# Kernel optimization log

Hardware: AMD Instinct MI355X
Metric: run time of the kernel (lower is better)

The kernel has to match this reference:

```python
import jax, jax.numpy as jnp
import numpy as np

B, C, H, W = 16, 256, 64, 64
NH, HD, NM = 4, 32, 4  # heads, head_dim, memory tokens
HID = NH * HD


def rms_norm(x, g):
    # F.normalize(x, dim=1) * sqrt(C) * g  (channel dim = 1)
    norm = jnp.maximum(jnp.linalg.norm(x, axis=1, keepdims=True), 1e-12)
    return x / norm * (x.shape[1] ** 0.5) * g


def setup_inputs() -> dict:
    key = jax.random.key(0)
    ks = jax.random.split(key, 5)
    return {
        "x": jax.random.normal(ks[0], (B, C, H, W), jnp.float32),
        "g_in": jnp.ones((1, C, 1, 1), jnp.float32),
        "mem_kv": jax.random.normal(ks[1], (2, NH, HD, NM), jnp.float32),
        "w_qkv": jax.random.normal(ks[2], (HID * 3, C), jnp.float32) * (C ** -0.5),
        "w_out": jax.random.normal(ks[3], (C, HID), jnp.float32) * (HID ** -0.5),
        "b_out": jnp.zeros((C,), jnp.float32),
        "g_out": jnp.ones((1, C, 1, 1), jnp.float32),
    }


def reference(x, g_in, mem_kv, w_qkv, w_out, b_out, g_out):
    b, c, h, w = x.shape
    n = h * w
    scale = HD ** -0.5

    xn = rms_norm(x, g_in)
    # 1x1 conv as matmul over channel dim: [B, 3*HID, H, W]
    qkv = jnp.einsum('oc,bchw->bohw', w_qkv, xn)
    q, k, v = jnp.split(qkv, 3, axis=1)
    # b (h d) x y -> b h d n
    q = q.reshape(b, NH, HD, n)
    k = k.reshape(b, NH, HD, n)
    v = v.reshape(b, NH, HD, n)

    # prepend memory key/value tokens: [b, h, d, NM + n]
    mk = jnp.broadcast_to(mem_kv[0], (b, NH, HD, NM))
    mv = jnp.broadcast_to(mem_kv[1], (b, NH, HD, NM))
    k = jnp.concatenate([mk, k], axis=-1)
    v = jnp.concatenate([mv, v], axis=-1)

    q = jax.nn.softmax(q, axis=-2) * scale  # softmax over head_dim
    k = jax.nn.softmax(k, axis=-1)          # softmax over tokens

    context = jnp.einsum('bhdn,bhen->bhde', k, v)  # [b, h, d, e]
    out = jnp.einsum('bhde,bhdn->bhen', context, q)  # [b, h, e, n]
    out = out.reshape(b, HID, h, w)

    out = jnp.einsum('oc,bchw->bohw', w_out, out) + b_out[None, :, None, None]
    return rms_norm(out, g_out)
```

## Files before the change

### kernel.cpp

```cpp
#include <hip/hip_runtime.h>
#include <math.h>

typedef unsigned short u16;
typedef unsigned int u32;

#define NBATCH 16
#define NCH    256
#define NPIX   4096
#define NHEAD  4
#define HDIM   32
#define NMEM   4
#define HID    128
#define OC3    384
#define SCALE_Q 0.17677669529663687f

typedef __bf16 bf16x8 __attribute__((ext_vector_type(8)));
typedef float  f32x4  __attribute__((ext_vector_type(4)));

__device__ __forceinline__ float bf2f(u16 u){ return __uint_as_float(((u32)u)<<16); }
__device__ __forceinline__ u16 bfb(float f){
  union { __bf16 h; u16 u; } x; x.h = (__bf16)f; return x.u;
}
__device__ __forceinline__ u32 pkbf2(float a, float b){
  union { __bf16 h[2]; u32 u; } x; x.h[0] = (__bf16)a; x.h[1] = (__bf16)b; return x.u;
}
__device__ __forceinline__ void unpack8(int4 v, float* o){
  u32 a=(u32)v.x, b=(u32)v.y, c=(u32)v.z, d=(u32)v.w;
  o[0]=__uint_as_float(a<<16); o[1]=__uint_as_float(a&0xffff0000u);
  o[2]=__uint_as_float(b<<16); o[3]=__uint_as_float(b&0xffff0000u);
  o[4]=__uint_as_float(c<<16); o[5]=__uint_as_float(c&0xffff0000u);
  o[6]=__uint_as_float(d<<16); o[7]=__uint_as_float(d&0xffff0000u);
}
__device__ __forceinline__ void gload_lds16(const void* gp, void* lp){
  __builtin_amdgcn_global_load_lds(
      (const __attribute__((address_space(1))) unsigned int*)gp,
      (__attribute__((address_space(3))) unsigned int*)lp, 16, 0, 0);
}

__global__ __launch_bounds__(256) void k_pack(const float* __restrict__ wqkv,
                                              const float* __restrict__ gin,
                                              const float* __restrict__ wout,
                                              u16* __restrict__ wqb,
                                              u16* __restrict__ wob)
{
  int i = blockIdx.x*256 + threadIdx.x;
  if (i < OC3*NCH){ int c = i & 255; wqb[i] = bfb(wqkv[i]*gin[c]); }
  else { int j = i - OC3*NCH; wob[j] = bfb(wout[j]); }
}

__global__ __launch_bounds__(512, 4) void k_qkvx(const float* __restrict__ x,
                                                 const u16* __restrict__ wqb,
                                                 u16* __restrict__ qt,
                                                 u16* __restrict__ kv)
{
  __shared__ __align__(16) char smem[52480];
  float (*Xs)[64]   = (float(*)[64])smem;
  u16*   Bx         = (u16*)(smem + 16384);
  float (*ssqp)[64] = (float(*)[64])(smem + 50176);
  float* rl         = (float*)(smem + 52224);
  float (*psx)[64]  = (float(*)[64])smem;

  const int t = threadIdx.x, w = t>>6, lane = t&63;
  const int n0 = blockIdx.x*64, b = blockIdx.y;
  const int qw = lane>>4, rr = lane&15;

  {
    float ssq = 0.f;
    for (int s=0;s<4;++s){
      asm volatile("s_waitcnt lgkmcnt(0)" ::: "memory");
      const float* gp = x + ((size_t)b*NCH + s*64 + w*8 + (lane>>4))*NPIX + n0 + (lane&15)*4;
      gload_lds16(gp,                    &Xs[w*8 + 0][0]);
      gload_lds16(gp + (size_t)4*NPIX,   &Xs[w*8 + 4][0]);
      asm volatile("s_waitcnt vmcnt(0)" ::: "memory");
      u32 pk[4];
      #pragma unroll
      for (int q=0;q<4;q++){
        float v0 = Xs[w*8 + 2*q    ][lane];
        float v1 = Xs[w*8 + 2*q + 1][lane];
        ssq += v0*v0 + v1*v1;
        pk[q] = pkbf2(v0, v1);
      }
      *(int4*)&Bx[lane*264 + s*64 + w*8] = make_int4((int)pk[0],(int)pk[1],(int)pk[2],(int)pk[3]);
    }
    ssqp[w][lane] = ssq;
  }
  __syncthreads();
  if (t < 64){
    float s = 0.f;
    #pragma unroll
    for (int g=0;g<8;g++) s += ssqp[g][t];
    rl[t] = 16.0f / fmaxf(sqrtf(s), 1e-12f);
  }

  f32x4 acc[3][4];
  #pragma unroll
  for (int p=0;p<3;p++)
    #pragma unroll
    for (int nf=0;nf<4;nf++) acc[p][nf] = (f32x4){0.f,0.f,0.f,0.f};

  const u16* aw = wqb + (size_t)(w*16 + rr)*NCH + qw*8;
  bf16x8 caf0 = *(const bf16x8*)(aw);
  bf16x8 caf1 = *(const bf16x8*)(aw + 128*NCH);
  bf16x8 caf2 = *(const bf16x8*)(aw + 256*NCH);
  #pragma unroll
  for (int c0=0; c0<NCH; c0+=32){
    bf16x8 bfr[4];
    #pragma unroll
    for (int nf=0;nf<4;nf++)
      bfr[nf] = *(const bf16x8*)&Bx[(nf*16+rr)*264 + c0 + qw*8];
    bf16x8 naf0 = caf0, naf1 = caf1, naf2 = caf2;
    if (c0 < NCH-32){
      naf0 = *(const bf16x8*)(aw + c0+32);
      naf1 = *(const bf16x8*)(aw + 128*NCH + c0+32);
      naf2 = *(const bf16x8*)(aw + 256*NCH + c0+32);
    }
    #pragma unroll
    for (int nf=0;nf<4;nf++){
      acc[0][nf] = __builtin_amdgcn_mfma_f32_16x16x32_bf16(caf0, bfr[nf], acc[0][nf], 0, 0, 0);
      acc[1][nf] = __builtin_amdgcn_mfma_f32_16x16x32_bf16(bfr[nf], caf1, acc[1][nf], 0, 0, 0);
      acc[2][nf] = __builtin_amdgcn_mfma_f32_16x16x32_bf16(bfr[nf], caf2, acc[2][nf], 0, 0, 0);
    }
    caf0 = naf0; caf1 = naf1; caf2 = naf2;
  }

  __syncthreads();

  #pragma unroll
  for (int p=1;p<3;p++){
    u16* base = kv + ((size_t)(b*256 + (p-1)*128 + w*16 + rr))*NPIX + n0;
    #pragma unroll
    for (int nf=0;nf<4;nf++){
      const float4 rv4 = *(const float4*)&rl[nf*16 + qw*4];
      u32 lo = pkbf2(acc[p][nf][0]*rv4.x, acc[p][nf][1]*rv4.y);
      u32 hi = pkbf2(acc[p][nf][2]*rv4.z, acc[p][nf][3]*rv4.w);
      *(int2*)(base + nf*16 + qw*4) = make_int2((int)lo,(int)hi);
    }
  }

  float qv[4][4], pm[4], ps[4];
  #pragma unroll
  for (int nf=0;nf<4;nf++){
    float rv = rl[nf*16 + rr];
    float m = -1e30f;
    #pragma unroll
    for (int r=0;r<4;r++){ qv[nf][r] = acc[0][nf][r]*rv; m = fmaxf(m, qv[nf][r]); }
    m = fmaxf(m, __shfl_xor(m, 16, 64));
    m = fmaxf(m, __shfl_xor(m, 32, 64));
    float s = 0.f;
    #pragma unroll
    for (int r=0;r<4;r++){ qv[nf][r] = __expf(qv[nf][r]-m); s += qv[nf][r]; }
    s += __shfl_xor(s, 16, 64);
    s += __shfl_xor(s, 32, 64);
    pm[nf] = m; ps[nf] = s;
  }
  if (lane < 16){
    #pragma unroll
    for (int nf=0;nf<4;nf++){ ssqp[w][nf*16+lane] = pm[nf]; psx[w][nf*16+lane] = ps[nf]; }
  }
  __syncthreads();
  {
    const int pw = w^1;
    u16* qbase = qt + ((size_t)b*NPIX + n0)*HID + w*16 + qw*4;
    #pragma unroll
    for (int nf=0;nf<4;nf++){
      float om = ssqp[pw][nf*16+rr], os = psx[pw][nf*16+rr];
      float M = fmaxf(pm[nf], om);
      float S = ps[nf]*__expf(pm[nf]-M) + os*__expf(om-M);
      float f = __expf(pm[nf]-M) * SCALE_Q / S;
      u32 lo = pkbf2(qv[nf][0]*f, qv[nf][1]*f);
      u32 hi = pkbf2(qv[nf][2]*f, qv[nf][3]*f);
      *(int2*)(qbase + (size_t)(nf*16+rr)*HID) = make_int2((int)lo,(int)hi);
    }
  }
}

__global__ __launch_bounds__(256) void k_kred(const u16* __restrict__ kv,
                                              const float* __restrict__ memkv,
                                              float2* __restrict__ kms,
                                              float* __restrict__ ksm)
{
  const int rid = blockIdx.x*4 + (threadIdx.x>>6);
  const int lane = threadIdx.x & 63;
  const int d = rid & 31, h = (rid>>5)&3, b = rid>>7;
  const u16* p = kv + (size_t)(b*256 + h*HDIM + d)*NPIX;
  u32 buf[32];
  #pragma unroll
  for (int j=0;j<8;j++)
    *(int4*)&buf[j*4] = *(const int4*)(p + (size_t)(j*64+lane)*8);
  float m = -1e30f;
  #pragma unroll
  for (int i=0;i<32;i++){
    float lo = __uint_as_float(buf[i]<<16);
    float hi = __uint_as_float(buf[i]&0xffff0000u);
    m = fmaxf(m, fmaxf(lo, hi));
  }
  float mv[4];
  #pragma unroll
  for (int mm=0;mm<4;mm++){ mv[mm] = memkv[(h*HDIM+d)*NMEM + mm]; m = fmaxf(m, mv[mm]); }
  #pragma unroll
  for (int sh=1; sh<64; sh<<=1) m = fmaxf(m, __shfl_xor(m, sh, 64));
  float ssum = 0.f;
  #pragma unroll
  for (int i=0;i<32;i++){
    float lo = __uint_as_float(buf[i]<<16);
    float hi = __uint_as_float(buf[i]&0xffff0000u);
    ssum += __expf(lo-m) + __expf(hi-m);
  }
  #pragma unroll
  for (int sh=1; sh<64; sh<<=1) ssum += __shfl_xor(ssum, sh, 64);
  #pragma unroll
  for (int mm=0;mm<4;mm++) ssum += __expf(mv[mm]-m);
  float inv = 1.0f/ssum;
  if (lane==0) kms[rid] = make_float2(m, inv);
  if (lane<4) ksm[rid*NMEM + lane] = __expf(mv[lane]-m)*inv;
}

__global__ __launch_bounds__(64) void k_ctx(const u16* __restrict__ kv,
                                            const float* __restrict__ memkv,
                                            const float* __restrict__ ksm,
                                            const float2* __restrict__ kms,
                                            float* __restrict__ ctxp)
{
  __shared__ float Ks[32][68];
  __shared__ float Vs[32][68];
  const int bh = blockIdx.x;
  const int s  = blockIdx.y;
  const int b = bh>>2, h = bh&3;
  const int t = threadIdx.x;
  const int d0 = (t>>3)*4, e0 = (t&7)*4;
  float acc[4][4] = {};
  if (s==0){
    #pragma unroll
    for (int m=0;m<4;m++){
      float km[4];
      #pragma unroll
      for (int pi=0;pi<4;pi++) km[pi] = ksm[(bh*HDIM + d0+pi)*NMEM + m];
      #pragma unroll
      for (int q=0;q<4;q++){
        float vm = memkv[((NHEAD+h)*HDIM + e0+q)*NMEM + m];
        #pragma unroll
        for (int pi=0;pi<4;pi++) acc[pi][q] += km[pi]*vm;
      }
    }
  }
  const u16* kb = kv + (size_t)(b*256 +       h*HDIM)*NPIX;
  const u16* vb = kv + (size_t)(b*256 + HID + h*HDIM)*NPIX;
  const int lr = t>>1, lseg = (t&1)*32;
  const float2 ms = kms[bh*HDIM + lr];
  #pragma unroll
  for (int half=0; half<2; ++half){
    const int n0 = s*128 + half*64;
    const u16* kp = kb + (size_t)lr*NPIX + n0 + lseg;
    const u16* vp = vb + (size_t)lr*NPIX + n0 + lseg;
    #pragma unroll
    for (int u=0;u<4;u++){
      int4 kvv = *(const int4*)(kp + u*8);
      int4 vv  = *(const int4*)(vp + u*8);
      float kf[8], vf[8];
      unpack8(kvv,kf); unpack8(vv,vf);
      #pragma unroll
      for (int i=0;i<8;i++) kf[i] = __expf(kf[i]-ms.x)*ms.y;
      *(float4*)&Ks[lr][lseg+u*8]   = make_float4(kf[0],kf[1],kf[2],kf[3]);
      *(float4*)&Ks[lr][lseg+u*8+4] = make_float4(kf[4],kf[5],kf[6],kf[7]);
      *(float4*)&Vs[lr][lseg+u*8]   = make_float4(vf[0],vf[1],vf[2],vf[3]);
      *(float4*)&Vs[lr][lseg+u*8+4] = make_float4(vf[4],vf[5],vf[6],vf[7]);
    }
    __syncthreads();
    #pragma unroll 4
    for (int nn=0;nn<64;nn+=4){
      float kq[4][4] __attribute__((aligned(16)));
      float vq[4][4] __attribute__((aligned(16)));
      #pragma unroll
      for (int pi=0;pi<4;pi++) *(float4*)kq[pi] = *(const float4*)&Ks[d0+pi][nn];
      #pragma unroll
      for (int q=0;q<4;q++)    *(float4*)vq[q]  = *(const float4*)&Vs[e0+q][nn];
      #pragma unroll
      for (int pi=0;pi<4;pi++)
        #pragma unroll
        for (int q=0;q<4;q++)
          acc[pi][q] += kq[pi][0]*vq[q][0] + kq[pi][1]*vq[q][1]
                      + kq[pi][2]*vq[q][2] + kq[pi][3]*vq[q][3];
    }
    __syncthreads();
  }
  #pragma unroll
  for (int pi=0;pi<4;pi++)
    *(float4*)(ctxp + (size_t)(s*64+bh)*1024 + (d0+pi)*32 + e0) =
      make_float4(acc[pi][0],acc[pi][1],acc[pi][2],acc[pi][3]);
}

__global__ __launch_bounds__(256) void k_ctxred(const float* __restrict__ ctxp,
                                                float* __restrict__ ctx)
{
  const int bh = blockIdx.x, t = threadIdx.x;
  float4 s = make_float4(0.f,0.f,0.f,0.f);
  #pragma unroll
  for (int sp=0; sp<32; sp++){
    float4 v = *(const float4*)(ctxp + (size_t)(sp*64+bh)*1024 + t*4);
    s.x+=v.x; s.y+=v.y; s.z+=v.z; s.w+=v.w;
  }
  *(float4*)(ctx + (size_t)bh*1024 + t*4) = s;
}

__global__ __launch_bounds__(256) void k_fout(const u16* __restrict__ qt,
                                              const float* __restrict__ ctx,
                                              const u16* __restrict__ wob,
                                              const float* __restrict__ bout,
                                              const float* __restrict__ gout,
                                              float* __restrict__ out)
{
  __shared__ u16 Cb[4*32*40];
  __shared__ u16 Ao[64*136];
  __shared__ float ssql[4][64];
  const int t = threadIdx.x, w = t>>6, lane = t&63;
  const int n0 = blockIdx.x*64, b = blockIdx.y;
  const int qw = lane>>4, rr = lane&15;

  {
    const float4* c4 = (const float4*)(ctx + (size_t)b*4096);
    const int d = (t>>3)&31, e0 = (t&7)*4;
    #pragma unroll
    for (int h=0;h<4;h++){
      float4 v = c4[t + h*256];
      Cb[(h*32+e0+0)*40 + d] = bfb(v.x);
      Cb[(h*32+e0+1)*40 + d] = bfb(v.y);
      Cb[(h*32+e0+2)*40 + d] = bfb(v.z);
      Cb[(h*32+e0+3)*40 + d] = bfb(v.w);
    }
  }
  __syncthreads();

  f32x4 pv[4][2];
  const u16* qp = qt + ((size_t)b*NPIX + n0 + w*16 + rr)*HID;
  #pragma unroll
  for (int h=0;h<4;h++){
    bf16x8 bq = *(const bf16x8*)(qp + h*32 + qw*8);
    #pragma unroll
    for (int ef=0;ef<2;ef++){
      bf16x8 af = *(const bf16x8*)&Cb[(h*32 + ef*16 + rr)*40 + qw*8];
      f32x4 z = (f32x4){0.f,0.f,0.f,0.f};
      pv[h][ef] = __builtin_amdgcn_mfma_f32_16x16x32_bf16(af, bq, z, 0, 0, 0);
    }
  }
  #pragma unroll
  for (int h=0;h<4;h++)
    #pragma unroll
    for (int ef=0;ef<2;ef++){
      u32 lohi0 = pkbf2(pv[h][ef][0], pv[h][ef][1]);
      u32 lohi1 = pkbf2(pv[h][ef][2], pv[h][ef][3]);
      *(int2*)&Ao[(w*16+rr)*136 + h*32 + ef*16 + qw*4] = make_int2((int)lohi0,(int)lohi1);
    }
  __syncthreads();

  f32x4 acc[4][4];
  #pragma unroll
  for (int i=0;i<4;i++)
    #pragma unroll
    for (int j=0;j<4;j++) acc[i][j] = (f32x4){0.f,0.f,0.f,0.f};
  #pragma unroll
  for (int k0=0; k0<HID; k0+=32){
    bf16x8 af[4], bfr[4];
    #pragma unroll
    for (int mf=0;mf<4;mf++)
      af[mf] = *(const bf16x8*)&wob[(size_t)(w*64 + mf*16 + rr)*HID + k0 + qw*8];
    #pragma unroll
    for (int nf=0;nf<4;nf++)
      bfr[nf] = *(const bf16x8*)&Ao[(nf*16+rr)*136 + k0 + qw*8];
    #pragma unroll
    for (int mf=0;mf<4;mf++)
      #pragma unroll
      for (int nf=0;nf<4;nf++)
        acc[mf][nf] = __builtin_amdgcn_mfma_f32_16x16x32_bf16(af[mf], bfr[nf], acc[mf][nf], 0, 0, 0);
  }
  float pssq[4] = {0.f,0.f,0.f,0.f};
  #pragma unroll
  for (int mf=0;mf<4;mf++)
    #pragma unroll
    for (int reg=0;reg<4;reg++){
      int c = w*64 + mf*16 + qw*4 + reg;
      float bb = bout[c];
      #pragma unroll
      for (int nf=0;nf<4;nf++){
        float v = acc[mf][nf][reg] + bb;
        acc[mf][nf][reg] = v;
        pssq[nf] += v*v;
      }
    }
  #pragma unroll
  for (int nf=0;nf<4;nf++){
    pssq[nf] += __shfl_xor(pssq[nf], 16, 64);
    pssq[nf] += __shfl_xor(pssq[nf], 32, 64);
  }
  if (qw==0){
    #pragma unroll
    for (int nf=0;nf<4;nf++) ssql[w][nf*16+rr] = pssq[nf];
  }
  __syncthreads();
  float rv[4];
  #pragma unroll
  for (int nf=0;nf<4;nf++){
    int col = nf*16 + rr;
    float sm = ssql[0][col]+ssql[1][col]+ssql[2][col]+ssql[3][col];
    rv[nf] = 16.0f / fmaxf(sqrtf(sm), 1e-12f);
  }
  #pragma unroll
  for (int mf=0;mf<4;mf++)
    #pragma unroll
    for (int reg=0;reg<4;reg++){
      int c = w*64 + mf*16 + qw*4 + reg;
      float g = gout[c];
      float* po = out + ((size_t)(b*NCH + c))*NPIX + n0;
      #pragma unroll
      for (int nf=0;nf<4;nf++)
        po[nf*16 + rr] = acc[mf][nf][reg]*rv[nf]*g;
    }
}

extern "C" void kernel_launch(void* const* d_in, const int* in_sizes, int n_in,
                              void* d_out, int out_size, void* d_ws, size_t ws_size,
                              hipStream_t stream)
{
  const float* x     = (const float*)d_in[0];
  const float* gin   = (const float*)d_in[1];
  const float* memkv = (const float*)d_in[2];
  const float* wqkv  = (const float*)d_in[3];
  const float* wout  = (const float*)d_in[4];
  const float* bout  = (const float*)d_in[5];
  const float* gout  = (const float*)d_in[6];
  float* out = (float*)d_out;

  char* ws = (char*)d_ws;
  u16*    kvb  = (u16*)   (ws);
  u16*    qt   = (u16*)   (ws + 33554432);
  float*  ksm  = (float*) (ws + 50331648);
  float2* kms  = (float2*)(ws + 50364416);
  float*  ctxp = (float*) (ws + 50380800);
  float*  ctx  = (float*) (ws + 58769408);
  u16*    wqb  = (u16*)   (ws + 59031552);
  u16*    wob  = (u16*)   (ws + 59228160);

  hipLaunchKernelGGL(k_pack,   dim3(512),   dim3(256), 0, stream, wqkv, gin, wout, wqb, wob);
  hipLaunchKernelGGL(k_qkvx,   dim3(64,16), dim3(512), 0, stream, x, wqb, qt, kvb);
  hipLaunchKernelGGL(k_kred,   dim3(512),   dim3(256), 0, stream, kvb, memkv, kms, ksm);
  hipLaunchKernelGGL(k_ctx,    dim3(64,32), dim3(64),  0, stream, kvb, memkv, ksm, kms, ctxp);
  hipLaunchKernelGGL(k_ctxred, dim3(64),    dim3(256), 0, stream, ctxp, ctx);
  hipLaunchKernelGGL(k_fout,   dim3(64,16), dim3(256), 0, stream, qt, ctx, wob, bout, gout, out);
}
```

Measured before the change: 198.7 us.

## Fuse key softmax and context accumulation into QKV projection kernel

The QKV kernel no longer writes K and V to global memory. It exponentiates K in-register without max subtraction, stores exp(K) and V tiles in LDS, and computes per-tile partial context with MFMA plus partial normalizer sums. A small finalize kernel then reduces the 64 partials per (batch, head), adds the memory tokens, and normalizes. This removes the 32MB bf16 K/V round trip and three separate kernels. The cost is extra LDS work and no max-stabilisation of exp, which can overflow on large logits.

```diff
diff --git a/kernel.cpp b/kernel.cpp
--- a/kernel.cpp
+++ b/kernel.cpp
@@ -17,19 +17,11 @@
 typedef __bf16 bf16x8 __attribute__((ext_vector_type(8)));
 typedef float  f32x4  __attribute__((ext_vector_type(4)));
 
-__device__ __forceinline__ float bf2f(u16 u){ return __uint_as_float(((u32)u)<<16); }
 __device__ __forceinline__ u16 bfb(float f){
   union { __bf16 h; u16 u; } x; x.h = (__bf16)f; return x.u;
 }
 __device__ __forceinline__ u32 pkbf2(float a, float b){
   union { __bf16 h[2]; u32 u; } x; x.h[0] = (__bf16)a; x.h[1] = (__bf16)b; return x.u;
-}
-__device__ __forceinline__ void unpack8(int4 v, float* o){
-  u32 a=(u32)v.x, b=(u32)v.y, c=(u32)v.z, d=(u32)v.w;
-  o[0]=__uint_as_float(a<<16); o[1]=__uint_as_float(a&0xffff0000u);
-  o[2]=__uint_as_float(b<<16); o[3]=__uint_as_float(b&0xffff0000u);
-  o[4]=__uint_as_float(c<<16); o[5]=__uint_as_float(c&0xffff0000u);
-  o[6]=__uint_as_float(d<<16); o[7]=__uint_as_float(d&0xffff0000u);
 }
 __device__ __forceinline__ void gload_lds16(const void* gp, void* lp){
   __builtin_amdgcn_global_load_lds(
@@ -51,14 +43,16 @@
 __global__ __launch_bounds__(512, 4) void k_qkvx(const float* __restrict__ x,
                                                  const u16* __restrict__ wqb,
                                                  u16* __restrict__ qt,
-                                                 u16* __restrict__ kv)
+                                                 float* __restrict__ ctxp2)
 {
   __shared__ __align__(16) char smem[52480];
   float (*Xs)[64]   = (float(*)[64])smem;
   u16*   Bx         = (u16*)(smem + 16384);
   float (*ssqp)[64] = (float(*)[64])(smem + 50176);
   float* rl         = (float*)(smem + 52224);
-  float (*psx)[64]  = (float(*)[64])smem;
+  u16*   Ek         = (u16*)smem;
+  u16*   Vv         = (u16*)(smem + 18432);
+  float (*psx)[64]  = (float(*)[64])(smem + 36864);
 
   const int t = threadIdx.x, w = t>>6, lane = t&63;
   const int n0 = blockIdx.x*64, b = blockIdx.y;
@@ -125,17 +119,24 @@
 
   __syncthreads();
 
-  #pragma unroll
-  for (int p=1;p<3;p++){
-    u16* base = kv + ((size_t)(b*256 + (p-1)*128 + w*16 + rr))*NPIX + n0;
-    #pragma unroll
-    for (int nf=0;nf<4;nf++){
-      const float4 rv4 = *(const float4*)&rl[nf*16 + qw*4];
-      u32 lo = pkbf2(acc[p][nf][0]*rv4.x, acc[p][nf][1]*rv4.y);
-      u32 hi = pkbf2(acc[p][nf][2]*rv4.z, acc[p][nf][3]*rv4.w);
-      *(int2*)(base + nf*16 + qw*4) = make_int2((int)lo,(int)hi);
-    }
-  }
+  float zk = 0.f;
+  #pragma unroll
+  for (int nf=0;nf<4;nf++){
+    const float4 rv4 = *(const float4*)&rl[nf*16 + qw*4];
+    float e0 = __expf(acc[1][nf][0]*rv4.x);
+    float e1 = __expf(acc[1][nf][1]*rv4.y);
+    float e2 = __expf(acc[1][nf][2]*rv4.z);
+    float e3 = __expf(acc[1][nf][3]*rv4.w);
+    zk += e0+e1+e2+e3;
+    *(int2*)&Ek[(w*16+rr)*72 + nf*16 + qw*4] =
+        make_int2((int)pkbf2(e0,e1), (int)pkbf2(e2,e3));
+    float v0 = acc[2][nf][0]*rv4.x, v1 = acc[2][nf][1]*rv4.y;
+    float v2 = acc[2][nf][2]*rv4.z, v3 = acc[2][nf][3]*rv4.w;
+    *(int2*)&Vv[(w*16+rr)*72 + nf*16 + qw*4] =
+        make_int2((int)pkbf2(v0,v1), (int)pkbf2(v2,v3));
+  }
+  zk += __shfl_xor(zk, 16, 64);
+  zk += __shfl_xor(zk, 32, 64);
 
   float qv[4][4], pm[4], ps[4];
   #pragma unroll
@@ -172,134 +173,55 @@
       *(int2*)(qbase + (size_t)(nf*16+rr)*HID) = make_int2((int)lo,(int)hi);
     }
   }
-}
-
-__global__ __launch_bounds__(256) void k_kred(const u16* __restrict__ kv,
-                                              const float* __restrict__ memkv,
-                                              float2* __restrict__ kms,
-                                              float* __restrict__ ksm)
-{
-  const int rid = blockIdx.x*4 + (threadIdx.x>>6);
-  const int lane = threadIdx.x & 63;
-  const int d = rid & 31, h = (rid>>5)&3, b = rid>>7;
-  const u16* p = kv + (size_t)(b*256 + h*HDIM + d)*NPIX;
-  u32 buf[32];
-  #pragma unroll
-  for (int j=0;j<8;j++)
-    *(int4*)&buf[j*4] = *(const int4*)(p + (size_t)(j*64+lane)*8);
-  float m = -1e30f;
-  #pragma unroll
-  for (int i=0;i<32;i++){
-    float lo = __uint_as_float(buf[i]<<16);
-    float hi = __uint_as_float(buf[i]&0xffff0000u);
-    m = fmaxf(m, fmaxf(lo, hi));
-  }
-  float mv[4];
-  #pragma unroll
-  for (int mm=0;mm<4;mm++){ mv[mm] = memkv[(h*HDIM+d)*NMEM + mm]; m = fmaxf(m, mv[mm]); }
-  #pragma unroll
-  for (int sh=1; sh<64; sh<<=1) m = fmaxf(m, __shfl_xor(m, sh, 64));
-  float ssum = 0.f;
-  #pragma unroll
-  for (int i=0;i<32;i++){
-    float lo = __uint_as_float(buf[i]<<16);
-    float hi = __uint_as_float(buf[i]&0xffff0000u);
-    ssum += __expf(lo-m) + __expf(hi-m);
-  }
-  #pragma unroll
-  for (int sh=1; sh<64; sh<<=1) ssum += __shfl_xor(ssum, sh, 64);
-  #pragma unroll
-  for (int mm=0;mm<4;mm++) ssum += __expf(mv[mm]-m);
-  float inv = 1.0f/ssum;
-  if (lane==0) kms[rid] = make_float2(m, inv);
-  if (lane<4) ksm[rid*NMEM + lane] = __expf(mv[lane]-m)*inv;
-}
-
-__global__ __launch_bounds__(64) void k_ctx(const u16* __restrict__ kv,
-                                            const float* __restrict__ memkv,
-                                            const float* __restrict__ ksm,
-                                            const float2* __restrict__ kms,
-                                            float* __restrict__ ctxp)
-{
-  __shared__ float Ks[32][68];
-  __shared__ float Vs[32][68];
-  const int bh = blockIdx.x;
-  const int s  = blockIdx.y;
-  const int b = bh>>2, h = bh&3;
-  const int t = threadIdx.x;
-  const int d0 = (t>>3)*4, e0 = (t&7)*4;
-  float acc[4][4] = {};
-  if (s==0){
-    #pragma unroll
-    for (int m=0;m<4;m++){
-      float km[4];
-      #pragma unroll
-      for (int pi=0;pi<4;pi++) km[pi] = ksm[(bh*HDIM + d0+pi)*NMEM + m];
-      #pragma unroll
-      for (int q=0;q<4;q++){
-        float vm = memkv[((NHEAD+h)*HDIM + e0+q)*NMEM + m];
-        #pragma unroll
-        for (int pi=0;pi<4;pi++) acc[pi][q] += km[pi]*vm;
+
+  {
+    const int h = w>>1, eh = w&1;
+    f32x4 pacc[2] = {(f32x4){0.f,0.f,0.f,0.f},(f32x4){0.f,0.f,0.f,0.f}};
+    #pragma unroll
+    for (int ks=0; ks<2; ks++){
+      bf16x8 bv = *(const bf16x8*)&Vv[(h*32+eh*16+rr)*72 + ks*32 + qw*8];
+      #pragma unroll
+      for (int i=0;i<2;i++){
+        bf16x8 ae = *(const bf16x8*)&Ek[(h*32+i*16+rr)*72 + ks*32 + qw*8];
+        pacc[i] = __builtin_amdgcn_mfma_f32_16x16x32_bf16(ae, bv, pacc[i], 0, 0, 0);
       }
     }
-  }
-  const u16* kb = kv + (size_t)(b*256 +       h*HDIM)*NPIX;
-  const u16* vb = kv + (size_t)(b*256 + HID + h*HDIM)*NPIX;
-  const int lr = t>>1, lseg = (t&1)*32;
-  const float2 ms = kms[bh*HDIM + lr];
-  #pragma unroll
-  for (int half=0; half<2; ++half){
-    const int n0 = s*128 + half*64;
-    const u16* kp = kb + (size_t)lr*NPIX + n0 + lseg;
-    const u16* vp = vb + (size_t)lr*NPIX + n0 + lseg;
-    #pragma unroll
-    for (int u=0;u<4;u++){
-      int4 kvv = *(const int4*)(kp + u*8);
-      int4 vv  = *(const int4*)(vp + u*8);
-      float kf[8], vf[8];
-      unpack8(kvv,kf); unpack8(vv,vf);
-      #pragma unroll
-      for (int i=0;i<8;i++) kf[i] = __expf(kf[i]-ms.x)*ms.y;
-      *(float4*)&Ks[lr][lseg+u*8]   = make_float4(kf[0],kf[1],kf[2],kf[3]);
-      *(float4*)&Ks[lr][lseg+u*8+4] = make_float4(kf[4],kf[5],kf[6],kf[7]);
-      *(float4*)&Vs[lr][lseg+u*8]   = make_float4(vf[0],vf[1],vf[2],vf[3]);
-      *(float4*)&Vs[lr][lseg+u*8+4] = make_float4(vf[4],vf[5],vf[6],vf[7]);
-    }
-    __syncthreads();
-    #pragma unroll 4
-    for (int nn=0;nn<64;nn+=4){
-      float kq[4][4] __attribute__((aligned(16)));
-      float vq[4][4] __attribute__((aligned(16)));
-      #pragma unroll
-      for (int pi=0;pi<4;pi++) *(float4*)kq[pi] = *(const float4*)&Ks[d0+pi][nn];
-      #pragma unroll
-      for (int q=0;q<4;q++)    *(float4*)vq[q]  = *(const float4*)&Vs[e0+q][nn];
-      #pragma unroll
-      for (int pi=0;pi<4;pi++)
-        #pragma unroll
-        for (int q=0;q<4;q++)
-          acc[pi][q] += kq[pi][0]*vq[q][0] + kq[pi][1]*vq[q][1]
-                      + kq[pi][2]*vq[q][2] + kq[pi][3]*vq[q][3];
-    }
-    __syncthreads();
-  }
-  #pragma unroll
-  for (int pi=0;pi<4;pi++)
-    *(float4*)(ctxp + (size_t)(s*64+bh)*1024 + (d0+pi)*32 + e0) =
-      make_float4(acc[pi][0],acc[pi][1],acc[pi][2],acc[pi][3]);
-}
-
-__global__ __launch_bounds__(256) void k_ctxred(const float* __restrict__ ctxp,
-                                                float* __restrict__ ctx)
-{
-  const int bh = blockIdx.x, t = threadIdx.x;
-  float4 s = make_float4(0.f,0.f,0.f,0.f);
-  #pragma unroll
-  for (int sp=0; sp<32; sp++){
-    float4 v = *(const float4*)(ctxp + (size_t)(sp*64+bh)*1024 + t*4);
-    s.x+=v.x; s.y+=v.y; s.z+=v.z; s.w+=v.w;
-  }
-  *(float4*)(ctx + (size_t)bh*1024 + t*4) = s;
+    float* pb = ctxp2 + ((size_t)((b*64 + blockIdx.x)*4 + h))*1088;
+    #pragma unroll
+    for (int i=0;i<2;i++)
+      #pragma unroll
+      for (int reg=0;reg<4;reg++)
+        pb[(i*16+qw*4+reg)*32 + eh*16 + rr] = pacc[i][reg];
+    if (qw==0) pb[1024 + (w&1)*16 + rr] = zk;
+  }
+}
+
+__global__ __launch_bounds__(256) void k_fin(const float* __restrict__ ctxp2,
+                                             const float* __restrict__ memkv,
+                                             float* __restrict__ ctx)
+{
+  const int bh = blockIdx.x, b = bh>>2, h = bh&3, t = threadIdx.x;
+  const int d = t>>3, e0 = (t&7)*4;
+  float4 ps = make_float4(0.f,0.f,0.f,0.f);
+  float z = 0.f;
+  for (int s=0;s<64;s++){
+    const float* pb = ctxp2 + ((size_t)((b*64+s)*4+h))*1088;
+    float4 v = *(const float4*)(pb + d*32 + e0);
+    ps.x+=v.x; ps.y+=v.y; ps.z+=v.z; ps.w+=v.w;
+    z += pb[1024 + d];
+  }
+  #pragma unroll
+  for (int m=0;m<4;m++){
+    float em = __expf(memkv[(h*HDIM+d)*NMEM + m]);
+    z += em;
+    ps.x += em*memkv[512 + (h*HDIM+e0+0)*NMEM + m];
+    ps.y += em*memkv[512 + (h*HDIM+e0+1)*NMEM + m];
+    ps.z += em*memkv[512 + (h*HDIM+e0+2)*NMEM + m];
+    ps.w += em*memkv[512 + (h*HDIM+e0+3)*NMEM + m];
+  }
+  float inv = 1.0f/z;
+  *(float4*)(ctx + (size_t)bh*1024 + d*32 + e0) =
+      make_float4(ps.x*inv, ps.y*inv, ps.z*inv, ps.w*inv);
 }
 
 __global__ __launch_bounds__(256) void k_fout(const u16* __restrict__ qt,
@@ -430,19 +352,13 @@
   float* out = (float*)d_out;
 
   char* ws = (char*)d_ws;
-  u16*    kvb  = (u16*)   (ws);
-  u16*    qt   = (u16*)   (ws + 33554432);
-  float*  ksm  = (float*) (ws + 50331648);
-  float2* kms  = (float2*)(ws + 50364416);
-  float*  ctxp = (float*) (ws + 50380800);
-  float*  ctx  = (float*) (ws + 58769408);
-  u16*    wqb  = (u16*)   (ws + 59031552);
-  u16*    wob  = (u16*)   (ws + 59228160);
-
-  hipLaunchKernelGGL(k_pack,   dim3(512),   dim3(256), 0, stream, wqkv, gin, wout, wqb, wob);
-  hipLaunchKernelGGL(k_qkvx,   dim3(64,16), dim3(512), 0, stream, x, wqb, qt, kvb);
-  hipLaunchKernelGGL(k_kred,   dim3(512),   dim3(256), 0, stream, kvb, memkv, kms, ksm);
-  hipLaunchKernelGGL(k_ctx,    dim3(64,32), dim3(64),  0, stream, kvb, memkv, ksm, kms, ctxp);
-  hipLaunchKernelGGL(k_ctxred, dim3(64),    dim3(256), 0, stream, ctxp, ctx);
-  hipLaunchKernelGGL(k_fout,   dim3(64,16), dim3(256), 0, stream, qt, ctx, wob, bout, gout, out);
-}
+  u16*    qt    = (u16*)   (ws);
+  float*  ctxp2 = (float*) (ws + 16777216);
+  float*  ctx   = (float*) (ws + 34603008);
+  u16*    wqb   = (u16*)   (ws + 34865152);
+  u16*    wob   = (u16*)   (ws + 35061760);
+  hipLaunchKernelGGL(k_pack, dim3(512),   dim3(256), 0, stream, wqkv, gin, wout, wqb, wob);
+  hipLaunchKernelGGL(k_qkvx, dim3(64,16), dim3(512), 0, stream, x, wqb, qt, ctxp2);
+  hipLaunchKernelGGL(k_fin,  dim3(64),    dim3(256), 0, stream, ctxp2, memkv, ctx);
+  hipLaunchKernelGGL(k_fout, dim3(64,16), dim3(256), 0, stream, qt, ctx, wob, bout, gout, out);
+}
```

New measurement: 172.5 us. -13.2%, faster.
